# Optimization experiments

Hardware: AMD Instinct MI355X
Metric: run time of the kernel (lower is better)

Reference implementation:

```python
import jax, jax.numpy as jnp
import numpy as np

B, T = 256, 20          # batch, sequence length
D = 128                 # encoder feature dim
H = 256                 # LSTM controller hidden / controller_output_size
KS = 256                # memory key/word size
MEM = 20                # memory slots
KNN = 4                 # k-NN addressing
Y = 4                   # output classes (y_dim)
EPS = 1e-8


def setup_inputs() -> dict:
    key = jax.random.key(0)
    ks = jax.random.split(key, 16)
    def kn(k, shape, fan_in):  # kaiming-normal-ish init
        return jax.random.normal(k, shape, jnp.float32) * np.float32(np.sqrt(2.0 / fan_in))
    return {
        "x": jax.random.normal(ks[0], (B, T, 32, 32), jnp.float32),
        # conv encoder
        "conv1_w": kn(ks[1], (32, 1, 4, 4), 1 * 16),  "conv1_b": jnp.zeros(32, jnp.float32),
        "conv2_w": kn(ks[2], (32, 32, 4, 4), 32 * 16), "conv2_b": jnp.zeros(32, jnp.float32),
        "conv3_w": kn(ks[3], (32, 32, 4, 4), 32 * 16), "conv3_b": jnp.zeros(32, jnp.float32),
        "fc1_w": kn(ks[4], (256, 512), 512), "fc1_b": jnp.zeros(256, jnp.float32),
        "fc2_w": kn(ks[5], (128, 256), 256), "fc2_b": jnp.zeros(128, jnp.float32),
        # context norm
        "gamma": jnp.ones(D, jnp.float32), "beta": jnp.zeros(D, jnp.float32),
        # LSTM controller: input = [z_t(128), read(256)] = 384
        "lstm_wi": kn(ks[6], (4 * H, D + KS), D + KS),
        "lstm_wh": kn(ks[7], (4 * H, H), H),
        "lstm_b": jnp.zeros(4 * H, jnp.float32),
        # head projections
        "wk": kn(ks[8], (KS, H), H),   # read key
        "wwk": kn(ks[9], (KS, H), H),  # write key
        "wv": kn(ks[10], (KS, H), H),  # write value
        # output layer on [h, read]
        "wo": kn(ks[11], (Y, H + KS), H + KS), "wo_b": jnp.zeros(Y, jnp.float32),
        "mem_init": jax.random.normal(ks[12], (MEM, KS), jnp.float32) * 0.01,
    }


def _conv(h, w, b):
    out = jax.lax.conv_general_dilated(h, w, (2, 2), [(1, 1), (1, 1)],
                                       dimension_numbers=("NCHW", "OIHW", "NCHW"))
    return jax.nn.relu(out + b[None, :, None, None])


def reference(x, conv1_w, conv1_b, conv2_w, conv2_b, conv3_w, conv3_b,
              fc1_w, fc1_b, fc2_w, fc2_b, gamma, beta,
              lstm_wi, lstm_wh, lstm_b, wk, wwk, wv, wo, wo_b, mem_init):
    b, t = x.shape[0], x.shape[1]
    # --- conv encoder on all B*T frames ---
    h = x.reshape(-1, 1, 32, 32)
    h = _conv(h, conv1_w, conv1_b)          # [BT,32,16,16]
    h = _conv(h, conv2_w, conv2_b)          # [BT,32,8,8]
    h = _conv(h, conv3_w, conv3_b)          # [BT,32,4,4]
    h = h.reshape(h.shape[0], -1)           # [BT,512] (NCHW flatten, matches torch)
    h = jax.nn.relu(h @ fc1_w.T + fc1_b)
    z = jax.nn.relu(h @ fc2_w.T + fc2_b).reshape(b, t, D)
    # --- context norm over time dim (torch var is unbiased) ---
    mu = z.mean(1)
    sigma = jnp.sqrt(z.var(1, ddof=1) + EPS)
    z = (z - mu[:, None, :]) / sigma[:, None, :] * gamma + beta
    # --- NTM-style MANN with k-NN addressing, scan over time ---
    zt = jnp.swapaxes(z, 0, 1)              # [T,B,D]
    M0 = jnp.broadcast_to(mem_init, (b, MEM, KS)) + jnp.zeros((b, MEM, KS), jnp.float32)
    carry0 = (jnp.zeros((b, H), jnp.float32), jnp.zeros((b, H), jnp.float32),
              jnp.zeros((b, KS), jnp.float32), M0)

    def step(carry, z_t):
        h_, c_, r_, M = carry
        inp = jnp.concatenate([z_t, r_], -1)
        gates = inp @ lstm_wi.T + h_ @ lstm_wh.T + lstm_b
        ig, fg, gg, og = jnp.split(gates, 4, -1)  # torch LSTM gate order i,f,g,o
        c_ = jax.nn.sigmoid(fg) * c_ + jax.nn.sigmoid(ig) * jnp.tanh(gg)
        h_ = jax.nn.sigmoid(og) * jnp.tanh(c_)
        Mn = M / (jnp.linalg.norm(M, axis=-1, keepdims=True) + EPS)
        def knn(kq):  # cosine sim -> top-k -> softmax weights
            kqn = kq / (jnp.linalg.norm(kq, axis=-1, keepdims=True) + EPS)
            sims = jnp.einsum('bd,bnd->bn', kqn, Mn)
            tv, ti = jax.lax.top_k(sims, KNN)
            return jax.nn.softmax(tv, -1), ti
        # read head
        wr, ir = knn(h_ @ wk.T)
        rows = jnp.take_along_axis(M, ir[..., None], axis=1)   # [B,KNN,KS] gather
        r_new = jnp.einsum('bk,bkd->bd', wr, rows)
        # write head: weighted scatter-add into top-k slots
        ws, iw = knn(h_ @ wwk.T)
        v = jnp.tanh(h_ @ wv.T)
        bidx = jnp.arange(M.shape[0])[:, None]
        M = M.at[bidx, iw].add(ws[..., None] * v[:, None, :])
        y = jnp.concatenate([h_, r_new], -1) @ wo.T + wo_b
        return (h_, c_, r_new, M), y

    _, ys = jax.lax.scan(step, carry0, zt)   # ys: [T,B,Y]
    y_pred_linear = ys[-1]
    return y_pred_linear, jnp.argmax(y_pred_linear, 1)
```

## Files before the change

kernel.cpp:

```cpp
#include <hip/hip_runtime.h>
#include <hip/hip_bf16.h>

#define EPSF 1e-8f

#define OFF_WIT 0
#define N_WIT   393216
#define OFF_WHT 393216
#define N_WHT   262144
#define OFF_PKT 655360
#define N_PKT   262144
#define OFF_F1T 917504
#define N_F1T   131072
#define OFF_F2T 1048576
#define N_F2T   32768
#define OFF_Z   1081344
#define N_Z     655360
#define WS_FLOATS 1736704

__global__ __launch_bounds__(256) void pack_kernel(
    const float* __restrict__ wi, const float* __restrict__ wh,
    const float* __restrict__ wk, const float* __restrict__ wwk,
    const float* __restrict__ wv,
    const float* __restrict__ f1w, const float* __restrict__ f2w,
    float* __restrict__ ws) {
  int id = blockIdx.x * 256 + threadIdx.x;
  if (id < N_WIT) {
    int k = id >> 10, r = id & 1023;
    ws[OFF_WIT + id] = wi[r * 384 + k];
    return;
  }
  id -= N_WIT;
  if (id < N_WHT) {
    int k = id >> 10, r = id & 1023;
    ws[OFF_WHT + id] = wh[r * 256 + k];
    return;
  }
  id -= N_WHT;
  if (id < N_PKT) {
    int m = id & 3, o = (id >> 2) & 255, k = id >> 10;
    float v = 0.f;
    if (m == 0) v = wk[o * 256 + k];
    else if (m == 1) v = wwk[o * 256 + k];
    else if (m == 2) v = wv[o * 256 + k];
    ws[OFF_PKT + id] = v;
    return;
  }
  id -= N_PKT;
  if (id < N_F1T) {
    int m = id & 3, o = (id >> 2) & 255, k4 = id >> 10;
    ws[OFF_F1T + id] = f1w[o * 512 + k4 * 4 + m];
    return;
  }
  id -= N_F1T;
  if (id < N_F2T) {
    int m = id & 3, o = (id >> 2) & 127, k4 = id >> 9;
    ws[OFF_F2T + id] = f2w[o * 256 + k4 * 4 + m];
  }
}

__global__ __launch_bounds__(256) void enc_kernel(
    const float* __restrict__ x,
    const float* __restrict__ w1, const float* __restrict__ b1,
    const float* __restrict__ w2, const float* __restrict__ b2,
    const float* __restrict__ w3, const float* __restrict__ b3,
    const float* __restrict__ f1b, const float* __restrict__ f2b,
    float* __restrict__ ws) {
  __shared__ __align__(16) float xs[1024];
  __shared__ __align__(16) float c1s[512 * 19];
  __shared__ __align__(16) float c2s[256 * 9];
  __shared__ __align__(16) float c3s[512];
  __shared__ __align__(16) float h1s[256];

  const float4* __restrict__ f1T4 = (const float4*)(ws + OFF_F1T);
  const float4* __restrict__ f2T4 = (const float4*)(ws + OFF_F2T);
  float* __restrict__ z = ws + OFF_Z;

  const int f = blockIdx.x;
  const int tid = threadIdx.x;

  for (int i = tid; i < 1024; i += 256) xs[i] = x[f * 1024 + i];
  __syncthreads();

  {
    int oy = tid >> 4, ox = tid & 15;
    float patch[16];
    #pragma unroll
    for (int ky = 0; ky < 4; ++ky) {
      int iy = oy * 2 - 1 + ky;
      #pragma unroll
      for (int kx = 0; kx < 4; ++kx) {
        int ix = ox * 2 - 1 + kx;
        patch[ky * 4 + kx] =
            ((unsigned)iy <= 31u && (unsigned)ix <= 31u) ? xs[iy * 32 + ix] : 0.f;
      }
    }
    for (int oc = 0; oc < 32; ++oc) {
      float acc = b1[oc];
      #pragma unroll
      for (int k = 0; k < 16; ++k) acc = fmaf(patch[k], w1[oc * 16 + k], acc);
      c1s[(oc * 16 + oy) * 19 + ox] = fmaxf(acc, 0.f);
    }
  }
  __syncthreads();

  {
    int pix = tid & 63;
    int og = __builtin_amdgcn_readfirstlane(tid >> 6);
    int oy = pix >> 3, ox = pix & 7;
    float acc[8];
    #pragma unroll
    for (int j = 0; j < 8; ++j) acc[j] = b2[og * 8 + j];
    for (int ic = 0; ic < 32; ++ic) {
      float patch[16];
      #pragma unroll
      for (int ky = 0; ky < 4; ++ky) {
        int iy = oy * 2 - 1 + ky;
        #pragma unroll
        for (int kx = 0; kx < 4; ++kx) {
          int ix = ox * 2 - 1 + kx;
          patch[ky * 4 + kx] = ((unsigned)iy <= 15u && (unsigned)ix <= 15u)
                                   ? c1s[(ic * 16 + iy) * 19 + ix] : 0.f;
        }
      }
      #pragma unroll
      for (int j = 0; j < 8; ++j) {
        const float* wr = w2 + ((og * 8 + j) * 32 + ic) * 16;
        #pragma unroll
        for (int k = 0; k < 16; ++k) acc[j] = fmaf(patch[k], wr[k], acc[j]);
      }
    }
    #pragma unroll
    for (int j = 0; j < 8; ++j)
      c2s[((og * 8 + j) * 8 + oy) * 9 + ox] = fmaxf(acc[j], 0.f);
  }
  __syncthreads();

  {
    int pix = tid & 15, grp = tid >> 4;
    int oy = pix >> 2, ox = pix & 3;
    float a0 = b3[grp * 2], a1 = b3[grp * 2 + 1];
    for (int ic = 0; ic < 32; ++ic) {
      float patch[16];
      #pragma unroll
      for (int ky = 0; ky < 4; ++ky) {
        int iy = oy * 2 - 1 + ky;
        #pragma unroll
        for (int kx = 0; kx < 4; ++kx) {
          int ix = ox * 2 - 1 + kx;
          patch[ky * 4 + kx] = ((unsigned)iy <= 7u && (unsigned)ix <= 7u)
                                   ? c2s[(ic * 8 + iy) * 9 + ix] : 0.f;
        }
      }
      const float4* wa = (const float4*)(w3 + ((grp * 2 + 0) * 32 + ic) * 16);
      const float4* wb = (const float4*)(w3 + ((grp * 2 + 1) * 32 + ic) * 16);
      #pragma unroll
      for (int q = 0; q < 4; ++q) {
        float4 qa = wa[q], qb = wb[q];
        a0 = fmaf(patch[q * 4 + 0], qa.x, a0);
        a0 = fmaf(patch[q * 4 + 1], qa.y, a0);
        a0 = fmaf(patch[q * 4 + 2], qa.z, a0);
        a0 = fmaf(patch[q * 4 + 3], qa.w, a0);
        a1 = fmaf(patch[q * 4 + 0], qb.x, a1);
        a1 = fmaf(patch[q * 4 + 1], qb.y, a1);
        a1 = fmaf(patch[q * 4 + 2], qb.z, a1);
        a1 = fmaf(patch[q * 4 + 3], qb.w, a1);
      }
    }
    c3s[(grp * 2 + 0) * 16 + pix] = fmaxf(a0, 0.f);
    c3s[(grp * 2 + 1) * 16 + pix] = fmaxf(a1, 0.f);
  }
  __syncthreads();

  {
    float acc = f1b[tid];
    for (int k4 = 0; k4 < 128; ++k4) {
      float4 cv = ((const float4*)c3s)[k4];
      float4 w = f1T4[k4 * 256 + tid];
      acc = fmaf(w.x, cv.x, acc);
      acc = fmaf(w.y, cv.y, acc);
      acc = fmaf(w.z, cv.z, acc);
      acc = fmaf(w.w, cv.w, acc);
    }
    h1s[tid] = fmaxf(acc, 0.f);
  }
  __syncthreads();

  if (tid < 128) {
    float acc = f2b[tid];
    for (int k4 = 0; k4 < 64; ++k4) {
      float4 hv = ((const float4*)h1s)[k4];
      float4 w = f2T4[k4 * 128 + tid];
      acc = fmaf(w.x, hv.x, acc);
      acc = fmaf(w.y, hv.y, acc);
      acc = fmaf(w.z, hv.z, acc);
      acc = fmaf(w.w, hv.w, acc);
    }
    z[f * 128 + tid] = fmaxf(acc, 0.f);
  }
}

__global__ __launch_bounds__(256) void norm_kernel(
    float* __restrict__ ws,
    const float* __restrict__ gamma, const float* __restrict__ beta) {
  float* z = ws + OFF_Z;
  int g = blockIdx.x * 256 + threadIdx.x;
  int b = g >> 7, d = g & 127;
  float vals[20];
  float mu = 0.f;
  #pragma unroll
  for (int t = 0; t < 20; ++t) {
    float v = z[(b * 20 + t) * 128 + d];
    vals[t] = v;
    mu += v;
  }
  mu *= (1.f / 20.f);
  float var = 0.f;
  #pragma unroll
  for (int t = 0; t < 20; ++t) {
    float dd = vals[t] - mu;
    var = fmaf(dd, dd, var);
  }
  var *= (1.f / 19.f);
  float inv = 1.f / sqrtf(var + EPSF);
  float ga = gamma[d], be = beta[d];
  #pragma unroll
  for (int t = 0; t < 20; ++t)
    z[(b * 20 + t) * 128 + d] = fmaf((vals[t] - mu) * inv, ga, be);
}

__global__ __launch_bounds__(256) void scan_kernel(
    const float* __restrict__ ws,
    const float* __restrict__ lb, const float* __restrict__ wo,
    const float* __restrict__ wob, const float* __restrict__ mem_init,
    float* __restrict__ out) {
  __shared__ float Msh[2][20 * 257];
  __shared__ __align__(16) float gsh[2][1024];
  __shared__ __align__(16) float inp[2][384];
  __shared__ __align__(16) float hsh[2][256];
  __shared__ float kq[2][2][256];
  __shared__ float vsh[2][256];
  __shared__ float sims[2][2][20];
  __shared__ float invq[2][2];
  __shared__ float wsel[2][2][4];
  __shared__ int isel[2][2][4];
  __shared__ float ysh[2][4];

  const int u = threadIdx.x;
  const int b0 = blockIdx.x * 2;
  const float4* wiT4 = (const float4*)(ws + OFF_WIT);
  const float4* whT4 = (const float4*)(ws + OFF_WHT);
  const float4* pkT4 = (const float4*)(ws + OFF_PKT);
  const float* zz = ws + OFF_Z;

  #pragma unroll
  for (int bl = 0; bl < 2; ++bl)
    for (int idx = u; idx < 5120; idx += 256)
      Msh[bl][(idx >> 8) * 257 + (idx & 255)] = mem_init[idx];
  hsh[0][u] = 0.f; hsh[1][u] = 0.f;
  inp[0][128 + u] = 0.f; inp[1][128 + u] = 0.f;
  float c0 = 0.f, c1 = 0.f;
  const float4 bias = ((const float4*)lb)[u];
  __syncthreads();

  for (int t = 0; t < 20; ++t) {
    if (u < 128) {
      inp[0][u] = zz[(b0 * 20 + t) * 128 + u];
      inp[1][u] = zz[((b0 + 1) * 20 + t) * 128 + u];
    }
    __syncthreads();

    float A0[4] = {bias.x, bias.y, bias.z, bias.w};
    float A1[4] = {bias.x, bias.y, bias.z, bias.w};
    for (int k4 = 0; k4 < 96; ++k4) {
      float4 i0 = ((const float4*)inp[0])[k4];
      float4 i1 = ((const float4*)inp[1])[k4];
      float f0[4] = {i0.x, i0.y, i0.z, i0.w};
      float f1[4] = {i1.x, i1.y, i1.z, i1.w};
      #pragma unroll
      for (int j = 0; j < 4; ++j) {
        float4 w = wiT4[(k4 * 4 + j) * 256 + u];
        A0[0] = fmaf(w.x, f0[j], A0[0]); A0[1] = fmaf(w.y, f0[j], A0[1]);
        A0[2] = fmaf(w.z, f0[j], A0[2]); A0[3] = fmaf(w.w, f0[j], A0[3]);
        A1[0] = fmaf(w.x, f1[j], A1[0]); A1[1] = fmaf(w.y, f1[j], A1[1]);
        A1[2] = fmaf(w.z, f1[j], A1[2]); A1[3] = fmaf(w.w, f1[j], A1[3]);
      }
    }
    for (int k4 = 0; k4 < 64; ++k4) {
      float4 h0 = ((const float4*)hsh[0])[k4];
      float4 h1 = ((const float4*)hsh[1])[k4];
      float f0[4] = {h0.x, h0.y, h0.z, h0.w};
      float f1[4] = {h1.x, h1.y, h1.z, h1.w};
      #pragma unroll
      for (int j = 0; j < 4; ++j) {
        float4 w = whT4[(k4 * 4 + j) * 256 + u];
        A0[0] = fmaf(w.x, f0[j], A0[0]); A0[1] = fmaf(w.y, f0[j], A0[1]);
        A0[2] = fmaf(w.z, f0[j], A0[2]); A0[3] = fmaf(w.w, f0[j], A0[3]);
        A1[0] = fmaf(w.x, f1[j], A1[0]); A1[1] = fmaf(w.y, f1[j], A1[1]);
        A1[2] = fmaf(w.z, f1[j], A1[2]); A1[3] = fmaf(w.w, f1[j], A1[3]);
      }
    }
    ((float4*)gsh[0])[u] = make_float4(A0[0], A0[1], A0[2], A0[3]);
    ((float4*)gsh[1])[u] = make_float4(A1[0], A1[1], A1[2], A1[3]);
    __syncthreads();

    {
      float i0 = gsh[0][u], fg0 = gsh[0][256 + u], g0 = gsh[0][512 + u], o0 = gsh[0][768 + u];
      float i1 = gsh[1][u], fg1 = gsh[1][256 + u], g1 = gsh[1][512 + u], o1 = gsh[1][768 + u];
      c0 = (1.f / (1.f + expf(-fg0))) * c0 + (1.f / (1.f + expf(-i0))) * tanhf(g0);
      c1 = (1.f / (1.f + expf(-fg1))) * c1 + (1.f / (1.f + expf(-i1))) * tanhf(g1);
      hsh[0][u] = (1.f / (1.f + expf(-o0))) * tanhf(c0);
      hsh[1][u] = (1.f / (1.f + expf(-o1))) * tanhf(c1);
    }
    __syncthreads();

    {
      float sk0 = 0.f, sk1 = 0.f, sw0 = 0.f, sw1 = 0.f, sv0 = 0.f, sv1 = 0.f;
      for (int k4 = 0; k4 < 64; ++k4) {
        float4 h0 = ((const float4*)hsh[0])[k4];
        float4 h1 = ((const float4*)hsh[1])[k4];
        float f0[4] = {h0.x, h0.y, h0.z, h0.w};
        float f1[4] = {h1.x, h1.y, h1.z, h1.w};
        #pragma unroll
        for (int j = 0; j < 4; ++j) {
          float4 w = pkT4[(k4 * 4 + j) * 256 + u];
          sk0 = fmaf(w.x, f0[j], sk0); sk1 = fmaf(w.x, f1[j], sk1);
          sw0 = fmaf(w.y, f0[j], sw0); sw1 = fmaf(w.y, f1[j], sw1);
          sv0 = fmaf(w.z, f0[j], sv0); sv1 = fmaf(w.z, f1[j], sv1);
        }
      }
      kq[0][0][u] = sk0; kq[0][1][u] = sw0; vsh[0][u] = tanhf(sv0);
      kq[1][0][u] = sk1; kq[1][1][u] = sw1; vsh[1][u] = tanhf(sv1);
    }
    __syncthreads();

    if (u < 160) {
      int n = u >> 3, l = u & 7;
      #pragma unroll
      for (int bl = 0; bl < 2; ++bl) {
        const float* Mr = &Msh[bl][n * 257];
        float ss = 0.f, s1 = 0.f, s2 = 0.f;
        for (int i = 0; i < 32; ++i) {
          int k = l + 8 * i;
          float m = Mr[k];
          ss = fmaf(m, m, ss);
          s1 = fmaf(kq[bl][0][k], m, s1);
          s2 = fmaf(kq[bl][1][k], m, s2);
        }
        ss += __shfl_xor(ss, 1); s1 += __shfl_xor(s1, 1); s2 += __shfl_xor(s2, 1);
        ss += __shfl_xor(ss, 2); s1 += __shfl_xor(s1, 2); s2 += __shfl_xor(s2, 2);
        ss += __shfl_xor(ss, 4); s1 += __shfl_xor(s1, 4); s2 += __shfl_xor(s2, 4);
        if (l == 0) {
          float inv = 1.f / (sqrtf(ss) + EPSF);
          sims[bl][0][n] = s1 * inv;
          sims[bl][1][n] = s2 * inv;
        }
      }
    } else if (u < 164) {
      int bl2 = (u - 160) >> 1, hd = u & 1;
      float qq = 0.f;
      for (int k = 0; k < 256; ++k) {
        float q = kq[bl2][hd][k];
        qq = fmaf(q, q, qq);
      }
      invq[bl2][hd] = 1.f / (sqrtf(qq) + EPSF);
    }
    __syncthreads();

    if (u < 4) {
      int bl = u >> 1, hd = u & 1;
      const float* sm = sims[bl][hd];
      float inv = invq[bl][hd];
      unsigned mask = 0;
      float tv[4];
      int ti[4];
      for (int j = 0; j < 4; ++j) {
        float best = -3.4e38f;
        int bx = 0;
        for (int n = 0; n < 20; ++n)
          if (!((mask >> n) & 1u) && sm[n] > best) { best = sm[n]; bx = n; }
        mask |= 1u << bx;
        tv[j] = best * inv;
        ti[j] = bx;
      }
      float e0 = 1.f;
      float e1 = expf(tv[1] - tv[0]);
      float e2 = expf(tv[2] - tv[0]);
      float e3 = expf(tv[3] - tv[0]);
      float s = e0 + e1 + e2 + e3;
      wsel[bl][hd][0] = e0 / s; wsel[bl][hd][1] = e1 / s;
      wsel[bl][hd][2] = e2 / s; wsel[bl][hd][3] = e3 / s;
      isel[bl][hd][0] = ti[0]; isel[bl][hd][1] = ti[1];
      isel[bl][hd][2] = ti[2]; isel[bl][hd][3] = ti[3];
    }
    __syncthreads();

    #pragma unroll
    for (int bl = 0; bl < 2; ++bl) {
      float rvv = 0.f;
      #pragma unroll
      for (int j = 0; j < 4; ++j)
        rvv = fmaf(wsel[bl][0][j], Msh[bl][isel[bl][0][j] * 257 + u], rvv);
      float vv = vsh[bl][u];
      #pragma unroll
      for (int j = 0; j < 4; ++j)
        Msh[bl][isel[bl][1][j] * 257 + u] += wsel[bl][1][j] * vv;
      inp[bl][128 + u] = rvv;
    }
    __syncthreads();
  }

  if (u < 8) {
    int bl = u >> 2, o = u & 3;
    float acc = wob[o];
    const float* wr = wo + o * 512;
    for (int k = 0; k < 256; ++k) acc = fmaf(wr[k], hsh[bl][k], acc);
    for (int k = 0; k < 256; ++k) acc = fmaf(wr[256 + k], inp[bl][128 + k], acc);
    ysh[bl][o] = acc;
    out[(b0 + bl) * 4 + o] = acc;
  }
  __syncthreads();
  if (u < 2) {
    float best = ysh[u][0];
    int bx = 0;
    #pragma unroll
    for (int o = 1; o < 4; ++o)
      if (ysh[u][o] > best) { best = ysh[u][o]; bx = o; }
    out[1024 + b0 + u] = (float)bx;
  }
}

__global__ __launch_bounds__(256) void fused_kernel(
    const float* __restrict__ x,
    const float* __restrict__ w1, const float* __restrict__ b1,
    const float* __restrict__ w2, const float* __restrict__ b2,
    const float* __restrict__ w3, const float* __restrict__ b3,
    const float* __restrict__ f1w, const float* __restrict__ f1b,
    const float* __restrict__ f2w, const float* __restrict__ f2b,
    const float* __restrict__ gamma, const float* __restrict__ beta,
    const float* __restrict__ wi, const float* __restrict__ wh,
    const float* __restrict__ lb, const float* __restrict__ wk,
    const float* __restrict__ wwk, const float* __restrict__ wv,
    const float* __restrict__ wo, const float* __restrict__ wob,
    const float* __restrict__ mem_init, float* __restrict__ out) {
  __shared__ float smem[15104];
  __shared__ float simr[20], simw[20], invq[2], wsel[2][4], ysh[4];
  __shared__ int isel[2][4];
  float* z_all = smem;
  float* pool = smem + 2560;
  float* xs = pool;
  float* c1s = pool + 1024;
  float* c2s = pool + 9216;
  float* c3s = pool + 11264;
  float* h1s = pool + 11776;
  float* w1s = pool + 12032;
  float* Msh = pool;
  float* inp = pool + 5140;
  float* hsh = pool + 5524;
  float* kqr = pool + 5780;
  float* kqw = pool + 6036;
  float* vsh = pool + 6292;
  const int tid = threadIdx.x;
  const int b = blockIdx.x;
  for (int i = tid; i < 512; i += 256) w1s[i] = w1[i];
  for (int f = 0; f < 20; ++f) {
    for (int i = tid; i < 1024; i += 256) xs[i] = x[(b * 20 + f) * 1024 + i];
    __syncthreads();
    for (int i = 0; i < 32; ++i) {
      int idx = i * 256 + tid;
      int oc = idx >> 8, pix = idx & 255, oy = pix >> 4, ox = pix & 15;
      float acc = b1[oc];
      for (int ky = 0; ky < 4; ++ky) {
        int iy = oy * 2 - 1 + ky;
        if ((unsigned)iy > 31u) continue;
        for (int kx = 0; kx < 4; ++kx) {
          int ix = ox * 2 - 1 + kx;
          if ((unsigned)ix > 31u) continue;
          acc = fmaf(xs[iy * 32 + ix], w1s[oc * 16 + ky * 4 + kx], acc);
        }
      }
      c1s[idx] = fmaxf(acc, 0.f);
    }
    __syncthreads();
    {
      int oc = tid >> 3, pg = tid & 7;
      float acc[8];
      float bb = b2[oc];
      for (int i = 0; i < 8; ++i) acc[i] = bb;
      for (int ic = 0; ic < 32; ++ic) {
        const float* in = &c1s[ic * 256];
        const float* wv_ = &w2[(oc * 32 + ic) * 16];
        for (int i = 0; i < 8; ++i) {
          int p = pg + 8 * i;
          int oy = p >> 3, ox = p & 7;
          for (int ky = 0; ky < 4; ++ky) {
            int iy = oy * 2 - 1 + ky;
            if ((unsigned)iy > 15u) continue;
            for (int kx = 0; kx < 4; ++kx) {
              int ix = ox * 2 - 1 + kx;
              if ((unsigned)ix > 15u) continue;
              acc[i] = fmaf(in[iy * 16 + ix], wv_[ky * 4 + kx], acc[i]);
            }
          }
        }
      }
      for (int i = 0; i < 8; ++i) c2s[oc * 64 + pg + 8 * i] = fmaxf(acc[i], 0.f);
    }
    __syncthreads();
    {
      int oc = tid >> 3, pg = tid & 7;
      float bb = b3[oc];
      float acc0 = bb, acc1 = bb;
      int p0 = pg, p1 = pg + 8;
      int oy0 = p0 >> 2, ox0 = p0 & 3, oy1 = p1 >> 2, ox1 = p1 & 3;
      for (int ic = 0; ic < 32; ++ic) {
        const float* in = &c2s[ic * 64];
        const float* wv_ = &w3[(oc * 32 + ic) * 16];
        for (int ky = 0; ky < 4; ++ky) {
          int iy0 = oy0 * 2 - 1 + ky, iy1 = oy1 * 2 - 1 + ky;
          for (int kx = 0; kx < 4; ++kx) {
            float w = wv_[ky * 4 + kx];
            int ix0 = ox0 * 2 - 1 + kx, ix1 = ox1 * 2 - 1 + kx;
            if ((unsigned)iy0 <= 7u && (unsigned)ix0 <= 7u)
              acc0 = fmaf(in[iy0 * 8 + ix0], w, acc0);
            if ((unsigned)iy1 <= 7u && (unsigned)ix1 <= 7u)
              acc1 = fmaf(in[iy1 * 8 + ix1], w, acc1);
          }
        }
      }
      c3s[oc * 16 + p0] = fmaxf(acc0, 0.f);
      c3s[oc * 16 + p1] = fmaxf(acc1, 0.f);
    }
    __syncthreads();
    {
      float acc = f1b[tid];
      const float* wr = f1w + tid * 512;
      for (int k = 0; k < 512; ++k) acc = fmaf(wr[k], c3s[k], acc);
      h1s[tid] = fmaxf(acc, 0.f);
    }
    __syncthreads();
    if (tid < 128) {
      float acc = f2b[tid];
      const float* wr = f2w + tid * 256;
      for (int k = 0; k < 256; ++k) acc = fmaf(wr[k], h1s[k], acc);
      z_all[f * 128 + tid] = fmaxf(acc, 0.f);
    }
    __syncthreads();
  }
  if (tid < 128) {
    float mu = 0.f;
    for (int t = 0; t < 20; ++t) mu += z_all[t * 128 + tid];
    mu *= (1.f / 20.f);
    float var = 0.f;
    for (int t = 0; t < 20; ++t) {
      float dd = z_all[t * 128 + tid] - mu;
      var = fmaf(dd, dd, var);
    }
    var *= (1.f / 19.f);
    float inv = 1.f / sqrtf(var + EPSF);
    float ga = gamma[tid], be = beta[tid];
    for (int t = 0; t < 20; ++t)
      z_all[t * 128 + tid] = fmaf((z_all[t * 128 + tid] - mu) * inv, ga, be);
  }
  for (int idx = tid; idx < 20 * 256; idx += 256)
    Msh[(idx >> 8) * 257 + (idx & 255)] = mem_init[idx];
  hsh[tid] = 0.f;
  inp[128 + tid] = 0.f;
  float c_reg = 0.f;
  __syncthreads();
  const int u = tid;
  for (int t = 0; t < 20; ++t) {
    if (u < 128) inp[u] = z_all[t * 128 + u];
    __syncthreads();
    float a[4];
    for (int g = 0; g < 4; ++g) {
      int row = g * 256 + u;
      float acc = lb[row];
      const float* wr = wi + row * 384;
      for (int k = 0; k < 384; ++k) acc = fmaf(wr[k], inp[k], acc);
      const float* hr = wh + row * 256;
      for (int k = 0; k < 256; ++k) acc = fmaf(hr[k], hsh[k], acc);
      a[g] = acc;
    }
    __syncthreads();
    {
      float ig = 1.f / (1.f + expf(-a[0]));
      float fg = 1.f / (1.f + expf(-a[1]));
      float gg = tanhf(a[2]);
      float og = 1.f / (1.f + expf(-a[3]));
      c_reg = fg * c_reg + ig * gg;
      hsh[u] = og * tanhf(c_reg);
    }
    __syncthreads();
    {
      float sk = 0.f, sw = 0.f, sv = 0.f;
      const float* rk = wk + u * 256;
      const float* rw = wwk + u * 256;
      const float* rv = wv + u * 256;
      for (int k = 0; k < 256; ++k) {
        float hv = hsh[k];
        sk = fmaf(rk[k], hv, sk);
        sw = fmaf(rw[k], hv, sw);
        sv = fmaf(rv[k], hv, sv);
      }
      kqr[u] = sk;
      kqw[u] = sw;
      vsh[u] = tanhf(sv);
    }
    __syncthreads();
    if (u < 20) {
      const float* Mr = &Msh[u * 257];
      float ss = 0.f, s1 = 0.f, s2 = 0.f;
      for (int k = 0; k < 256; ++k) {
        float m = Mr[k];
        ss = fmaf(m, m, ss);
        s1 = fmaf(kqr[k], m, s1);
        s2 = fmaf(kqw[k], m, s2);
      }
      float inv = 1.f / (sqrtf(ss) + EPSF);
      simr[u] = s1 * inv;
      simw[u] = s2 * inv;
    } else if (u == 20 || u == 21) {
      const float* q = (u == 20) ? kqr : kqw;
      float qq = 0.f;
      for (int k = 0; k < 256; ++k) qq = fmaf(q[k], q[k], qq);
      invq[u - 20] = 1.f / (sqrtf(qq) + EPSF);
    }
    __syncthreads();
    if (u < 2) {
      const float* sims = (u == 0) ? simr : simw;
      float inv = invq[u];
      unsigned mask = 0;
      float tv[4];
      int ti[4];
      for (int j = 0; j < 4; ++j) {
        float best = -3.4e38f;
        int bx = 0;
        for (int n = 0; n < 20; ++n)
          if (!((mask >> n) & 1u) && sims[n] > best) { best = sims[n]; bx = n; }
        mask |= 1u << bx;
        tv[j] = best * inv;
        ti[j] = bx;
      }
      float e1 = expf(tv[1] - tv[0]);
      float e2 = expf(tv[2] - tv[0]);
      float e3 = expf(tv[3] - tv[0]);
      float s = 1.f + e1 + e2 + e3;
      wsel[u][0] = 1.f / s; wsel[u][1] = e1 / s; wsel[u][2] = e2 / s; wsel[u][3] = e3 / s;
      isel[u][0] = ti[0]; isel[u][1] = ti[1]; isel[u][2] = ti[2]; isel[u][3] = ti[3];
    }
    __syncthreads();
    {
      float rvv = 0.f;
      for (int j = 0; j < 4; ++j)
        rvv = fmaf(wsel[0][j], Msh[isel[0][j] * 257 + u], rvv);
      float vv = vsh[u];
      for (int j = 0; j < 4; ++j)
        Msh[isel[1][j] * 257 + u] += wsel[1][j] * vv;
      inp[128 + u] = rvv;
    }
    __syncthreads();
  }
  if (u < 4) {
    float acc = wob[u];
    const float* wr = wo + u * 512;
    for (int k = 0; k < 256; ++k) acc = fmaf(wr[k], hsh[k], acc);
    for (int k = 0; k < 256; ++k) acc = fmaf(wr[256 + k], inp[128 + k], acc);
    ysh[u] = acc;
    out[b * 4 + u] = acc;
  }
  __syncthreads();
  if (u == 0) {
    float best = ysh[0];
    int bx = 0;
    for (int o = 1; o < 4; ++o)
      if (ysh[o] > best) { best = ysh[o]; bx = o; }
    out[1024 + b] = (float)bx;
  }
}

extern "C" void kernel_launch(void* const* d_in, const int* in_sizes, int n_in,
                              void* d_out, int out_size, void* d_ws, size_t ws_size,
                              hipStream_t stream) {
  const float* x    = (const float*)d_in[0];
  const float* c1w  = (const float*)d_in[1];
  const float* c1b  = (const float*)d_in[2];
  const float* c2w  = (const float*)d_in[3];
  const float* c2b  = (const float*)d_in[4];
  const float* c3w  = (const float*)d_in[5];
  const float* c3b  = (const float*)d_in[6];
  const float* f1w  = (const float*)d_in[7];
  const float* f1b  = (const float*)d_in[8];
  const float* f2w  = (const float*)d_in[9];
  const float* f2b  = (const float*)d_in[10];
  const float* gam  = (const float*)d_in[11];
  const float* bet  = (const float*)d_in[12];
  const float* wi   = (const float*)d_in[13];
  const float* wh   = (const float*)d_in[14];
  const float* lb   = (const float*)d_in[15];
  const float* wk   = (const float*)d_in[16];
  const float* wwk  = (const float*)d_in[17];
  const float* wv   = (const float*)d_in[18];
  const float* wo   = (const float*)d_in[19];
  const float* wob  = (const float*)d_in[20];
  const float* mem0 = (const float*)d_in[21];
  float* out = (float*)d_out;

  if (ws_size >= (size_t)WS_FLOATS * sizeof(float)) {
    float* ws = (float*)d_ws;
    pack_kernel<<<4224, 256, 0, stream>>>(wi, wh, wk, wwk, wv, f1w, f2w, ws);
    enc_kernel<<<5120, 256, 0, stream>>>(x, c1w, c1b, c2w, c2b, c3w, c3b,
                                         f1b, f2b, ws);
    norm_kernel<<<128, 256, 0, stream>>>(ws, gam, bet);
    scan_kernel<<<128, 256, 0, stream>>>(ws, lb, wo, wob, mem0, out);
  } else {
    fused_kernel<<<256, 256, 0, stream>>>(x, c1w, c1b, c2w, c2b, c3w, c3b,
                                          f1w, f1b, f2w, f2b, gam, bet,
                                          wi, wh, lb, wk, wwk, wv, wo, wob,
                                          mem0, out);
  }
}
```

Measured before the change: 1.330 ms.

## Widen scan kernel to 1024 threads with one gate row per thread

The sequential scan kernel now runs 1024 threads per block instead of 256. Each thread computes one LSTM gate row and each head-projection thread computes one output of the three heads, replacing per-thread float4 gate tiles. The packed head-weight layout drops the zero padding slot, which shrinks the workspace and the pack grid. This aims to cut per-step latency of the serial recurrence by spreading the matvec across more wavefronts. In exchange the weight loads become scalar instead of float4, and barriers now span more waves.

New measurement: 1.347 ms. Within noise of the previous version (+1.3%).

```diff
diff --git a/kernel.cpp b/kernel.cpp
--- a/kernel.cpp
+++ b/kernel.cpp
@@ -8,14 +8,14 @@
 #define OFF_WHT 393216
 #define N_WHT   262144
 #define OFF_PKT 655360
-#define N_PKT   262144
-#define OFF_F1T 917504
+#define N_PKT   196608
+#define OFF_F1T 851968
 #define N_F1T   131072
-#define OFF_F2T 1048576
+#define OFF_F2T 983040
 #define N_F2T   32768
-#define OFF_Z   1081344
+#define OFF_Z   1015808
 #define N_Z     655360
-#define WS_FLOATS 1736704
+#define WS_FLOATS 1671168
 
 __global__ __launch_bounds__(256) void pack_kernel(
     const float* __restrict__ wi, const float* __restrict__ wh,
@@ -37,11 +37,10 @@
   }
   id -= N_WHT;
   if (id < N_PKT) {
-    int m = id & 3, o = (id >> 2) & 255, k = id >> 10;
-    float v = 0.f;
-    if (m == 0) v = wk[o * 256 + k];
-    else if (m == 1) v = wwk[o * 256 + k];
-    else if (m == 2) v = wv[o * 256 + k];
+    int k = id / 768, c = id % 768;
+    int m = c >> 8, o = c & 255;
+    float v = (m == 0) ? wk[o * 256 + k] : (m == 1) ? wwk[o * 256 + k]
+                                                     : wv[o * 256 + k];
     ws[OFF_PKT + id] = v;
     return;
   }
@@ -228,7 +227,7 @@
     z[(b * 20 + t) * 128 + d] = fmaf((vals[t] - mu) * inv, ga, be);
 }
 
-__global__ __launch_bounds__(256) void scan_kernel(
+__global__ __launch_bounds__(1024) void scan_kernel(
     const float* __restrict__ ws,
     const float* __restrict__ lb, const float* __restrict__ wo,
     const float* __restrict__ wob, const float* __restrict__ mem_init,
@@ -237,7 +236,7 @@
   __shared__ __align__(16) float gsh[2][1024];
   __shared__ __align__(16) float inp[2][384];
   __shared__ __align__(16) float hsh[2][256];
-  __shared__ float kq[2][2][256];
+  __shared__ float kqsh[2][2][256];
   __shared__ float vsh[2][256];
   __shared__ float sims[2][2][20];
   __shared__ float invq[2][2];
@@ -245,129 +244,136 @@
   __shared__ int isel[2][2][4];
   __shared__ float ysh[2][4];
 
-  const int u = threadIdx.x;
+  const int r = threadIdx.x;
   const int b0 = blockIdx.x * 2;
-  const float4* wiT4 = (const float4*)(ws + OFF_WIT);
-  const float4* whT4 = (const float4*)(ws + OFF_WHT);
-  const float4* pkT4 = (const float4*)(ws + OFF_PKT);
+  const float* wiT = ws + OFF_WIT;
+  const float* whT = ws + OFF_WHT;
+  const float* pkT = ws + OFF_PKT;
   const float* zz = ws + OFF_Z;
 
   #pragma unroll
   for (int bl = 0; bl < 2; ++bl)
-    for (int idx = u; idx < 5120; idx += 256)
+    for (int idx = r; idx < 5120; idx += 1024)
       Msh[bl][(idx >> 8) * 257 + (idx & 255)] = mem_init[idx];
-  hsh[0][u] = 0.f; hsh[1][u] = 0.f;
-  inp[0][128 + u] = 0.f; inp[1][128 + u] = 0.f;
-  float c0 = 0.f, c1 = 0.f;
-  const float4 bias = ((const float4*)lb)[u];
+  if (r < 512) {
+    int bl = r >> 8, u = r & 255;
+    hsh[bl][u] = 0.f;
+    inp[bl][128 + u] = 0.f;
+  }
+  float c_reg = 0.f;
+  const float bias = lb[r];
   __syncthreads();
 
   for (int t = 0; t < 20; ++t) {
-    if (u < 128) {
-      inp[0][u] = zz[(b0 * 20 + t) * 128 + u];
-      inp[1][u] = zz[((b0 + 1) * 20 + t) * 128 + u];
-    }
-    __syncthreads();
-
-    float A0[4] = {bias.x, bias.y, bias.z, bias.w};
-    float A1[4] = {bias.x, bias.y, bias.z, bias.w};
-    for (int k4 = 0; k4 < 96; ++k4) {
-      float4 i0 = ((const float4*)inp[0])[k4];
-      float4 i1 = ((const float4*)inp[1])[k4];
-      float f0[4] = {i0.x, i0.y, i0.z, i0.w};
-      float f1[4] = {i1.x, i1.y, i1.z, i1.w};
-      #pragma unroll
-      for (int j = 0; j < 4; ++j) {
-        float4 w = wiT4[(k4 * 4 + j) * 256 + u];
-        A0[0] = fmaf(w.x, f0[j], A0[0]); A0[1] = fmaf(w.y, f0[j], A0[1]);
-        A0[2] = fmaf(w.z, f0[j], A0[2]); A0[3] = fmaf(w.w, f0[j], A0[3]);
-        A1[0] = fmaf(w.x, f1[j], A1[0]); A1[1] = fmaf(w.y, f1[j], A1[1]);
-        A1[2] = fmaf(w.z, f1[j], A1[2]); A1[3] = fmaf(w.w, f1[j], A1[3]);
-      }
-    }
-    for (int k4 = 0; k4 < 64; ++k4) {
-      float4 h0 = ((const float4*)hsh[0])[k4];
-      float4 h1 = ((const float4*)hsh[1])[k4];
-      float f0[4] = {h0.x, h0.y, h0.z, h0.w};
-      float f1[4] = {h1.x, h1.y, h1.z, h1.w};
-      #pragma unroll
-      for (int j = 0; j < 4; ++j) {
-        float4 w = whT4[(k4 * 4 + j) * 256 + u];
-        A0[0] = fmaf(w.x, f0[j], A0[0]); A0[1] = fmaf(w.y, f0[j], A0[1]);
-        A0[2] = fmaf(w.z, f0[j], A0[2]); A0[3] = fmaf(w.w, f0[j], A0[3]);
-        A1[0] = fmaf(w.x, f1[j], A1[0]); A1[1] = fmaf(w.y, f1[j], A1[1]);
-        A1[2] = fmaf(w.z, f1[j], A1[2]); A1[3] = fmaf(w.w, f1[j], A1[3]);
-      }
-    }
-    ((float4*)gsh[0])[u] = make_float4(A0[0], A0[1], A0[2], A0[3]);
-    ((float4*)gsh[1])[u] = make_float4(A1[0], A1[1], A1[2], A1[3]);
-    __syncthreads();
-
+    if (r < 256) {
+      int bl = r >> 7, d = r & 127;
+      inp[bl][d] = zz[((b0 + bl) * 20 + t) * 128 + d];
+    }
+    __syncthreads();
+
+    float a0 = bias, a1 = bias;
     {
-      float i0 = gsh[0][u], fg0 = gsh[0][256 + u], g0 = gsh[0][512 + u], o0 = gsh[0][768 + u];
-      float i1 = gsh[1][u], fg1 = gsh[1][256 + u], g1 = gsh[1][512 + u], o1 = gsh[1][768 + u];
-      c0 = (1.f / (1.f + expf(-fg0))) * c0 + (1.f / (1.f + expf(-i0))) * tanhf(g0);
-      c1 = (1.f / (1.f + expf(-fg1))) * c1 + (1.f / (1.f + expf(-i1))) * tanhf(g1);
-      hsh[0][u] = (1.f / (1.f + expf(-o0))) * tanhf(c0);
-      hsh[1][u] = (1.f / (1.f + expf(-o1))) * tanhf(c1);
-    }
-    __syncthreads();
-
-    {
-      float sk0 = 0.f, sk1 = 0.f, sw0 = 0.f, sw1 = 0.f, sv0 = 0.f, sv1 = 0.f;
+      const float4* ip0 = (const float4*)inp[0];
+      const float4* ip1 = (const float4*)inp[1];
+      for (int k4 = 0; k4 < 96; ++k4) {
+        float4 z0 = ip0[k4], z1 = ip1[k4];
+        float w0 = wiT[(k4 * 4 + 0) * 1024 + r];
+        float w1 = wiT[(k4 * 4 + 1) * 1024 + r];
+        float w2 = wiT[(k4 * 4 + 2) * 1024 + r];
+        float w3 = wiT[(k4 * 4 + 3) * 1024 + r];
+        a0 = fmaf(w0, z0.x, a0); a1 = fmaf(w0, z1.x, a1);
+        a0 = fmaf(w1, z0.y, a0); a1 = fmaf(w1, z1.y, a1);
+        a0 = fmaf(w2, z0.z, a0); a1 = fmaf(w2, z1.z, a1);
+        a0 = fmaf(w3, z0.w, a0); a1 = fmaf(w3, z1.w, a1);
+      }
+      const float4* hp0 = (const float4*)hsh[0];
+      const float4* hp1 = (const float4*)hsh[1];
       for (int k4 = 0; k4 < 64; ++k4) {
-        float4 h0 = ((const float4*)hsh[0])[k4];
-        float4 h1 = ((const float4*)hsh[1])[k4];
-        float f0[4] = {h0.x, h0.y, h0.z, h0.w};
-        float f1[4] = {h1.x, h1.y, h1.z, h1.w};
-        #pragma unroll
-        for (int j = 0; j < 4; ++j) {
-          float4 w = pkT4[(k4 * 4 + j) * 256 + u];
-          sk0 = fmaf(w.x, f0[j], sk0); sk1 = fmaf(w.x, f1[j], sk1);
-          sw0 = fmaf(w.y, f0[j], sw0); sw1 = fmaf(w.y, f1[j], sw1);
-          sv0 = fmaf(w.z, f0[j], sv0); sv1 = fmaf(w.z, f1[j], sv1);
-        }
-      }
-      kq[0][0][u] = sk0; kq[0][1][u] = sw0; vsh[0][u] = tanhf(sv0);
-      kq[1][0][u] = sk1; kq[1][1][u] = sw1; vsh[1][u] = tanhf(sv1);
-    }
-    __syncthreads();
-
-    if (u < 160) {
-      int n = u >> 3, l = u & 7;
-      #pragma unroll
-      for (int bl = 0; bl < 2; ++bl) {
-        const float* Mr = &Msh[bl][n * 257];
-        float ss = 0.f, s1 = 0.f, s2 = 0.f;
-        for (int i = 0; i < 32; ++i) {
-          int k = l + 8 * i;
-          float m = Mr[k];
-          ss = fmaf(m, m, ss);
-          s1 = fmaf(kq[bl][0][k], m, s1);
-          s2 = fmaf(kq[bl][1][k], m, s2);
-        }
-        ss += __shfl_xor(ss, 1); s1 += __shfl_xor(s1, 1); s2 += __shfl_xor(s2, 1);
-        ss += __shfl_xor(ss, 2); s1 += __shfl_xor(s1, 2); s2 += __shfl_xor(s2, 2);
-        ss += __shfl_xor(ss, 4); s1 += __shfl_xor(s1, 4); s2 += __shfl_xor(s2, 4);
-        if (l == 0) {
-          float inv = 1.f / (sqrtf(ss) + EPSF);
-          sims[bl][0][n] = s1 * inv;
-          sims[bl][1][n] = s2 * inv;
-        }
-      }
-    } else if (u < 164) {
-      int bl2 = (u - 160) >> 1, hd = u & 1;
+        float4 h0 = hp0[k4], h1 = hp1[k4];
+        float w0 = whT[(k4 * 4 + 0) * 1024 + r];
+        float w1 = whT[(k4 * 4 + 1) * 1024 + r];
+        float w2 = whT[(k4 * 4 + 2) * 1024 + r];
+        float w3 = whT[(k4 * 4 + 3) * 1024 + r];
+        a0 = fmaf(w0, h0.x, a0); a1 = fmaf(w0, h1.x, a1);
+        a0 = fmaf(w1, h0.y, a0); a1 = fmaf(w1, h1.y, a1);
+        a0 = fmaf(w2, h0.z, a0); a1 = fmaf(w2, h1.z, a1);
+        a0 = fmaf(w3, h0.w, a0); a1 = fmaf(w3, h1.w, a1);
+      }
+    }
+    gsh[0][r] = a0;
+    gsh[1][r] = a1;
+    __syncthreads();
+
+    if (r < 512) {
+      int bl = r >> 8, u = r & 255;
+      float ig = gsh[bl][u], fg = gsh[bl][256 + u];
+      float gg = gsh[bl][512 + u], og = gsh[bl][768 + u];
+      c_reg = (1.f / (1.f + expf(-fg))) * c_reg +
+              (1.f / (1.f + expf(-ig))) * tanhf(gg);
+      hsh[bl][u] = (1.f / (1.f + expf(-og))) * tanhf(c_reg);
+    }
+    __syncthreads();
+
+    if (r < 768) {
+      int m = r >> 8, o = r & 255;
+      float s0 = 0.f, s1 = 0.f;
+      const float4* hp0 = (const float4*)hsh[0];
+      const float4* hp1 = (const float4*)hsh[1];
+      for (int k4 = 0; k4 < 64; ++k4) {
+        float4 h0 = hp0[k4], h1 = hp1[k4];
+        float w0 = pkT[(k4 * 4 + 0) * 768 + r];
+        float w1 = pkT[(k4 * 4 + 1) * 768 + r];
+        float w2 = pkT[(k4 * 4 + 2) * 768 + r];
+        float w3 = pkT[(k4 * 4 + 3) * 768 + r];
+        s0 = fmaf(w0, h0.x, s0); s1 = fmaf(w0, h1.x, s1);
+        s0 = fmaf(w1, h0.y, s0); s1 = fmaf(w1, h1.y, s1);
+        s0 = fmaf(w2, h0.z, s0); s1 = fmaf(w2, h1.z, s1);
+        s0 = fmaf(w3, h0.w, s0); s1 = fmaf(w3, h1.w, s1);
+      }
+      if (m < 2) {
+        kqsh[0][m][o] = s0;
+        kqsh[1][m][o] = s1;
+      } else {
+        vsh[0][o] = tanhf(s0);
+        vsh[1][o] = tanhf(s1);
+      }
+    }
+    __syncthreads();
+
+    if (r < 320) {
+      int bl = r >= 160;
+      int q = bl ? r - 160 : r;
+      int n = q >> 3, l = q & 7;
+      const float* Mr = &Msh[bl][n * 257];
+      float ss = 0.f, s1 = 0.f, s2 = 0.f;
+      for (int i = 0; i < 32; ++i) {
+        int k = l + 8 * i;
+        float m = Mr[k];
+        ss = fmaf(m, m, ss);
+        s1 = fmaf(kqsh[bl][0][k], m, s1);
+        s2 = fmaf(kqsh[bl][1][k], m, s2);
+      }
+      ss += __shfl_xor(ss, 1); s1 += __shfl_xor(s1, 1); s2 += __shfl_xor(s2, 1);
+      ss += __shfl_xor(ss, 2); s1 += __shfl_xor(s1, 2); s2 += __shfl_xor(s2, 2);
+      ss += __shfl_xor(ss, 4); s1 += __shfl_xor(s1, 4); s2 += __shfl_xor(s2, 4);
+      if (l == 0) {
+        float inv = 1.f / (sqrtf(ss) + EPSF);
+        sims[bl][0][n] = s1 * inv;
+        sims[bl][1][n] = s2 * inv;
+      }
+    } else if (r < 324) {
+      int bl2 = (r - 320) >> 1, hd = r & 1;
       float qq = 0.f;
       for (int k = 0; k < 256; ++k) {
-        float q = kq[bl2][hd][k];
+        float q = kqsh[bl2][hd][k];
         qq = fmaf(q, q, qq);
       }
       invq[bl2][hd] = 1.f / (sqrtf(qq) + EPSF);
     }
     __syncthreads();
 
-    if (u < 4) {
-      int bl = u >> 1, hd = u & 1;
+    if (r < 4) {
+      int bl = r >> 1, hd = r & 1;
       const float* sm = sims[bl][hd];
       float inv = invq[bl][hd];
       unsigned mask = 0;
@@ -394,8 +400,8 @@
     }
     __syncthreads();
 
-    #pragma unroll
-    for (int bl = 0; bl < 2; ++bl) {
+    if (r < 512) {
+      int bl = r >> 8, u = r & 255;
       float rvv = 0.f;
       #pragma unroll
       for (int j = 0; j < 4; ++j)
@@ -409,8 +415,8 @@
     __syncthreads();
   }
 
-  if (u < 8) {
-    int bl = u >> 2, o = u & 3;
+  if (r < 8) {
+    int bl = r >> 2, o = r & 3;
     float acc = wob[o];
     const float* wr = wo + o * 512;
     for (int k = 0; k < 256; ++k) acc = fmaf(wr[k], hsh[bl][k], acc);
@@ -419,13 +425,13 @@
     out[(b0 + bl) * 4 + o] = acc;
   }
   __syncthreads();
-  if (u < 2) {
-    float best = ysh[u][0];
+  if (r < 2) {
+    float best = ysh[r][0];
     int bx = 0;
     #pragma unroll
     for (int o = 1; o < 4; ++o)
-      if (ysh[u][o] > best) { best = ysh[u][o]; bx = o; }
-    out[1024 + b0 + u] = (float)bx;
+      if (ysh[r][o] > best) { best = ysh[r][o]; bx = o; }
+    out[1024 + b0 + r] = (float)bx;
   }
 }
 
@@ -707,11 +713,11 @@
 
   if (ws_size >= (size_t)WS_FLOATS * sizeof(float)) {
     float* ws = (float*)d_ws;
-    pack_kernel<<<4224, 256, 0, stream>>>(wi, wh, wk, wwk, wv, f1w, f2w, ws);
+    pack_kernel<<<3968, 256, 0, stream>>>(wi, wh, wk, wwk, wv, f1w, f2w, ws);
     enc_kernel<<<5120, 256, 0, stream>>>(x, c1w, c1b, c2w, c2b, c3w, c3b,
                                          f1b, f2b, ws);
     norm_kernel<<<128, 256, 0, stream>>>(ws, gam, bet);
-    scan_kernel<<<128, 256, 0, stream>>>(ws, lb, wo, wob, mem0, out);
+    scan_kernel<<<128, 1024, 0, stream>>>(ws, lb, wo, wob, mem0, out);
   } else {
     fused_kernel<<<256, 256, 0, stream>>>(x, c1w, c1b, c2w, c2b, c3w, c3b,
                                           f1w, f1b, f2w, f2b, gam, bet,
```
